# Kernel tuning notes

Measured on AMD Instinct MI355X. Metric: run time of the kernel, lower is better.

Reference implementation:

```python
import math
import jax, jax.numpy as jnp
import numpy as np

M, D, NL, H, DFF = 14, 128, 2, 4, 512
BS = 256
DK = D // H


def setup_inputs() -> dict:
    key = jax.random.key(0)
    ks = iter(jax.random.split(key, 40))
    def w(shape, s=0.02):
        return jax.random.normal(next(ks), shape, jnp.float32) * s
    return dict(
        src=jax.random.normal(next(ks), (BS, M), jnp.float32),
        t=5,
        fc_w=w((D, 1, 3), 0.3), fc_b=jnp.zeros((D,), jnp.float32),
        gc_w=w((D, 1, 3), 0.3), gc_b=jnp.zeros((D,), jnp.float32),
        ln_w=jnp.ones((D,), jnp.float32), ln_b=jnp.zeros((D,), jnp.float32),
        qw=w((NL, D, D)), qb=jnp.zeros((NL, D), jnp.float32),
        kw=w((NL, D, D)), kb=jnp.zeros((NL, D), jnp.float32),
        vw=w((NL, D, D)), vb=jnp.zeros((NL, D), jnp.float32),
        ow=w((NL, D, D)), ob=jnp.zeros((NL, D), jnp.float32),
        n1a=jnp.ones((NL, D), jnp.float32), n1b=jnp.zeros((NL, D), jnp.float32),
        n2a=jnp.ones((NL, D), jnp.float32), n2b=jnp.zeros((NL, D), jnp.float32),
        w1=w((NL, DFF, D)), b1=jnp.zeros((NL, DFF), jnp.float32),
        w2=w((NL, D, DFF)), b2=jnp.zeros((NL, D), jnp.float32),
        fna=jnp.ones((D,), jnp.float32), fnb=jnp.zeros((D,), jnp.float32),
        out_w=w((1, D)), out_b=jnp.zeros((1,), jnp.float32),
    )


def _conv1d(x, w):  # x [B,1,m], w [O,1,3], padding=1 (SAME)
    return jax.lax.conv_general_dilated(
        x, w, window_strides=(1,), padding=[(1, 1)],
        dimension_numbers=('NCH', 'OIH', 'NCH'))


def _norm(x, a, b, eps=1e-6):
    # torch: alpha*(x-mean)/(std+eps)+bias, std is UNBIASED (ddof=1)
    mu = x.mean(-1, keepdims=True)
    std = jnp.sqrt(jnp.var(x, axis=-1, ddof=1, keepdims=True))
    return a * (x - mu) / (std + eps) + b


def _mha(x, qw, qb, kw, kb, vw, vb, ow, ob):
    bs = x.shape[0]
    def proj(w, b):  # view(bs,-1,h,dk).transpose(1,2) -> [bs,h,s,dk]
        return jnp.swapaxes((x @ w.T + b).reshape(bs, -1, H, DK), 1, 2)
    q, k, v = proj(qw, qb), proj(kw, kb), proj(vw, vb)
    scores = jax.nn.softmax(
        jnp.einsum('bhqd,bhkd->bhqk', q, k) / math.sqrt(DK), axis=-1)
    o = jnp.einsum('bhqk,bhkd->bhqd', scores, v)
    o = jnp.swapaxes(o, 1, 2).reshape(bs, -1, D)
    return o @ ow.T + ob


def _forward(src, fc_w, fc_b, gc_w, gc_b, ln_w, ln_b, qw, qb, kw, kb, vw, vb,
             ow, ob, n1a, n1b, n2a, n2b, w1, b1, w2, b2, fna, fnb,
             out_w, out_b, t):
    # --- GCU embedding: gated conv over the m features, pooled to [bs, D]
    xc = src[:, None, :]                                 # [bs,1,m]
    feat = _conv1d(xc, fc_w) + fc_b[None, :, None]        # [bs,D,m]
    gate = jax.nn.sigmoid(_conv1d(xc, gc_w) + gc_b[None, :, None])
    g = (feat * gate).mean(-1)                            # adaptive_avg_pool1d(.,1)
    mu = g.mean(-1, keepdims=True)                        # torch LayerNorm (biased var)
    var = ((g - mu) ** 2).mean(-1, keepdims=True)
    x = ln_w * (g - mu) / jnp.sqrt(var + 1e-5) + ln_b     # [bs,D]
    # --- positional encoding with scalar position t
    div = jnp.exp(jnp.arange(0, D, 2, dtype=jnp.float32) * (-math.log(10000.0) / D))
    pe = jnp.zeros((D,), jnp.float32).at[0::2].set(jnp.sin(t * div)).at[1::2].set(jnp.cos(t * div))
    x = x * math.sqrt(D) + pe
    # --- encoder layers (layer 0 broadcast-promotes x to [bs,bs,D], faithful to torch)
    for i in range(NL):
        x2 = _norm(x, n1a[i], n1b[i])
        x = x + _mha(x2, qw[i], qb[i], kw[i], kb[i], vw[i], vb[i], ow[i], ob[i])
        x2 = _norm(x, n2a[i], n2b[i])
        x = x + (jax.nn.relu(x2 @ w1[i].T + b1[i]) @ w2[i].T + b2[i])
    x = _norm(x, fna, fnb)
    out = x @ out_w.T + out_b                             # [bs,bs,1]
    return out.squeeze(-1)                                # [bs,bs]


def reference(src, fc_w, fc_b, gc_w, gc_b, ln_w, ln_b, qw, qb, kw, kb, vw, vb,
              ow, ob, n1a, n1b, n2a, n2b, w1, b1, w2, b2, fna, fnb,
              out_w, out_b, t):
    return _forward(src, fc_w, fc_b, gc_w, gc_b, ln_w, ln_b, qw, qb, kw, kb,
                    vw, vb, ow, ob, n1a, n1b, n2a, n2b, w1, b1, w2, b2,
                    fna, fnb, out_w, out_b, t)
```

## Files before the change

### kernel.cpp

```cpp
#include <hip/hip_runtime.h>
#include <math.h>


#define SQRT_D 11.313708498984761f
#define PE_C   0.14391156831212787f
#define INV_SQRT_DK 0.17677669529663687f
#define XF(j,d) (((j) << 7) + ((d) ^ (((j) & 15) << 2)))

typedef _Float16 f16x8 __attribute__((ext_vector_type(8)));
typedef float    f32x4 __attribute__((ext_vector_type(4)));

#define MFMA(a, b, c) __builtin_amdgcn_mfma_f32_16x16x32_f16((a), (b), (c), 0, 0, 0)

__device__ __forceinline__ unsigned pack2(float a, float b) {
  union { _Float16 h; unsigned short s; } ua, ub;
  ua.h = (_Float16)a; ub.h = (_Float16)b;
  return (unsigned)ua.s | ((unsigned)ub.s << 16);
}

__device__ __forceinline__ unsigned bperm(int addr, unsigned v) {
  return (unsigned)__builtin_amdgcn_ds_bpermute(addr, (int)v);
}

__device__ __forceinline__ f16x8 u4f16x8(unsigned u0, unsigned u1, unsigned u2, unsigned u3) {
  union { unsigned u[4]; f16x8 f; } x;
  x.u[0] = u0; x.u[1] = u1; x.u[2] = u2; x.u[3] = u3;
  return x.f;
}

__device__ __forceinline__ f16x8 make_bfrag(f32x4 cA, f32x4 cB, int aLo, int aHi, int hiSel) {
  unsigned a0 = pack2(cA[0], cA[1]), a1 = pack2(cA[2], cA[3]);
  unsigned b0 = pack2(cB[0], cB[1]), b1 = pack2(cB[2], cB[3]);
  unsigned lA0 = bperm(aLo, a0), lA1 = bperm(aLo, a1);
  unsigned hA0 = bperm(aHi, a0), hA1 = bperm(aHi, a1);
  unsigned lB0 = bperm(aLo, b0), lB1 = bperm(aLo, b1);
  unsigned hB0 = bperm(aHi, b0), hB1 = bperm(aHi, b1);
  return u4f16x8(hiSel ? lB0 : lA0, hiSel ? lB1 : lA1,
                 hiSel ? hB0 : hA0, hiSel ? hB1 : hA1);
}

struct P0 { const float *qw, *kw, *vw, *ow, *w1, *w2; _Float16* dst; };

__global__ __launch_bounds__(256) void convf16(P0 p) {
  const int idx = blockIdx.x * 256 + threadIdx.x;
  float v;
  if      (idx <  32768) v = p.qw[idx];
  else if (idx <  65536) v = p.kw[idx -  32768];
  else if (idx <  98304) v = p.vw[idx -  65536];
  else if (idx < 131072) v = p.ow[idx -  98304];
  else if (idx < 262144) v = p.w1[idx - 131072];
  else                   v = p.w2[idx - 262144];
  p.dst[idx] = (_Float16)v;
}

struct P1 {
  const float* src; const int* t;
  const float* fc_w; const float* fc_b; const float* gc_w; const float* gc_b;
  const float* ln_w; const float* ln_b;
  const float* n1a; const float* n1b;
  const float* vw; const float* vb; const float* ow; const float* ob;
  float* x0; float* a0;
};

__device__ __forceinline__ float rowReduceSum(float v, volatile float* red, int d) {
#pragma unroll
  for (int off = 32; off > 0; off >>= 1) v += __shfl_xor(v, off, 64);
  if ((d & 63) == 0) red[d >> 6] = v;
  __syncthreads();
  float r = red[0] + red[1];
  __syncthreads();
  return r;
}

__device__ __forceinline__ float dot128s(const float* __restrict__ w,
                                         const float* __restrict__ xs) {
  const float4* __restrict__ w4 = (const float4*)w;
  const float4* __restrict__ x4 = (const float4*)xs;
  float a0 = 0.f, a1 = 0.f, a2 = 0.f, a3 = 0.f;
#pragma unroll
  for (int k = 0; k < 32; k += 4) {
    float4 xv0 = x4[k + 0], xv1 = x4[k + 1], xv2 = x4[k + 2], xv3 = x4[k + 3];
    float4 wv0 = w4[k + 0], wv1 = w4[k + 1], wv2 = w4[k + 2], wv3 = w4[k + 3];
    a0 = fmaf(wv0.w, xv0.w, fmaf(wv0.z, xv0.z, fmaf(wv0.y, xv0.y, fmaf(wv0.x, xv0.x, a0))));
    a1 = fmaf(wv1.w, xv1.w, fmaf(wv1.z, xv1.z, fmaf(wv1.y, xv1.y, fmaf(wv1.x, xv1.x, a1))));
    a2 = fmaf(wv2.w, xv2.w, fmaf(wv2.z, xv2.z, fmaf(wv2.y, xv2.y, fmaf(wv2.x, xv2.x, a2))));
    a3 = fmaf(wv3.w, xv3.w, fmaf(wv3.z, xv3.z, fmaf(wv3.y, xv3.y, fmaf(wv3.x, xv3.x, a3))));
  }
  return (a0 + a1) + (a2 + a3);
}

__global__ __launch_bounds__(256) void prep(P1 p) {
  __shared__ __align__(16) float s_src[2][16];
  __shared__ __align__(16) float s_x2[2][128];
  __shared__ __align__(16) float s_y[2][128];
  __shared__ float s_red[2][2];

  const int tid = threadIdx.x;
  const int rl  = tid >> 7;
  const int d   = tid & 127;
  const int row = blockIdx.x * 2 + rl;
  volatile float* red = s_red[rl];

  if (d < 14) s_src[rl][d + 1] = p.src[row * 14 + d];
  if (d == 14) { s_src[rl][0] = 0.f; s_src[rl][15] = 0.f; }
  __syncthreads();

  const float fw0 = p.fc_w[3*d+0], fw1 = p.fc_w[3*d+1], fw2 = p.fc_w[3*d+2];
  const float gw0 = p.gc_w[3*d+0], gw1 = p.gc_w[3*d+1], gw2 = p.gc_w[3*d+2];
  const float fb = p.fc_b[d], gb = p.gc_b[d];
  float g = 0.f;
#pragma unroll
  for (int m = 0; m < 14; ++m) {
    float xm1 = s_src[rl][m], x0v = s_src[rl][m+1], xp1 = s_src[rl][m+2];
    float f  = fmaf(fw2, xp1, fmaf(fw1, x0v, fmaf(fw0, xm1, fb)));
    float ga = fmaf(gw2, xp1, fmaf(gw1, x0v, fmaf(gw0, xm1, gb)));
    g = fmaf(f, 1.f / (1.f + expf(-ga)), g);
  }
  g *= (1.f / 14.f);

  float mu = rowReduceSum(g, red, d) * (1.f / 128.f);
  float cg = g - mu;
  float var = rowReduceSum(cg * cg, red, d) * (1.f / 128.f);
  float x = fmaf(p.ln_w[d], cg * rsqrtf(var + 1e-5f), p.ln_b[d]);

  const int tval = *p.t;
  {
    int i2 = d >> 1;
    float arg = (float)tval * expf((float)i2 * -PE_C);
    float pe = (d & 1) ? cosf(arg) : sinf(arg);
    x = fmaf(x, SQRT_D, pe);
  }
  p.x0[row * 128 + d] = x;

  float mu1 = rowReduceSum(x, red, d) * (1.f / 128.f);
  float c1 = x - mu1;
  float v1 = rowReduceSum(c1 * c1, red, d) * (1.f / 127.f);
  s_x2[rl][d] = fmaf(p.n1a[d], c1 / (sqrtf(v1) + 1e-6f), p.n1b[d]);
  __syncthreads();

  float y = p.vb[d] + dot128s(p.vw + d * 128, s_x2[rl]);
  s_y[rl][d] = y;
  __syncthreads();
  p.a0[row * 128 + d] = p.ob[d] + dot128s(p.ow + d * 128, s_y[rl]);
}

struct P2 {
  const float* x0; const float* a0;
  const _Float16 *wq, *wk, *wvv, *wo, *w1h, *w2h;
  const float *qb, *kb, *vb, *ob;
  const float *n1a, *n1b, *n2a, *n2b;
  const float *b1, *b2;
  const float *fna, *fnb, *out_w, *out_b;
  float* out;
};

__device__ __forceinline__ void build_x2_pass(const float* sX, int strip, int nt, int l,
    const float* __restrict__ na, const float* __restrict__ nb, f16x8 out[4]) {
  const int l15 = l & 15, q = l >> 4;
  const int row = strip + nt * 16 + l15;
  float sum = 0.f, sq = 0.f;
#pragma unroll
  for (int c4 = 0; c4 < 8; ++c4) {
    f32x4 v = *(const f32x4*)&sX[XF(row, q * 32 + c4 * 4)];
#pragma unroll
    for (int e = 0; e < 4; ++e) { sum += v[e]; sq = fmaf(v[e], v[e], sq); }
  }
  sum += __shfl_xor(sum, 16); sum += __shfl_xor(sum, 32);
  sq  += __shfl_xor(sq, 16);  sq  += __shfl_xor(sq, 32);
  const float mu = sum * (1.f / 128.f);
  const float var = fmaf(-sum, mu, sq) * (1.f / 127.f);
  const float inv = 1.f / (sqrtf(var) + 1e-6f);
#pragma unroll
  for (int kt = 0; kt < 4; ++kt) {
    const int d0 = kt * 32 + q * 8;
    f32x4 xA = *(const f32x4*)&sX[XF(row, d0)];
    f32x4 xB = *(const f32x4*)&sX[XF(row, d0 + 4)];
    f32x4 nA = *(const f32x4*)&na[d0], nB = *(const f32x4*)&na[d0 + 4];
    f32x4 bA = *(const f32x4*)&nb[d0], bB = *(const f32x4*)&nb[d0 + 4];
    float v0 = fmaf(nA[0] * inv, xA[0] - mu, bA[0]);
    float v1 = fmaf(nA[1] * inv, xA[1] - mu, bA[1]);
    float v2 = fmaf(nA[2] * inv, xA[2] - mu, bA[2]);
    float v3 = fmaf(nA[3] * inv, xA[3] - mu, bA[3]);
    float v4 = fmaf(nB[0] * inv, xB[0] - mu, bB[0]);
    float v5 = fmaf(nB[1] * inv, xB[1] - mu, bB[1]);
    float v6 = fmaf(nB[2] * inv, xB[2] - mu, bB[2]);
    float v7 = fmaf(nB[3] * inv, xB[3] - mu, bB[3]);
    out[kt] = u4f16x8(pack2(v0, v1), pack2(v2, v3), pack2(v4, v5), pack2(v6, v7));
  }
}

__device__ __forceinline__ void ffn_phase(float* sX, _Float16* aux, int t,
    int strip, int l, const float* __restrict__ na, const float* __restrict__ nb,
    const _Float16* __restrict__ w1, const float* __restrict__ b1,
    const _Float16* __restrict__ w2, const float* __restrict__ b2,
    int aLo, int aHi, int hiSel) {
  const int l15 = l & 15, lg = l >> 4;
  f16x8 x2f[4][2];
#pragma unroll
  for (int nt = 0; nt < 2; ++nt) {
    f16x8 tmp[4];
    build_x2_pass(sX, strip, nt, l, na, nb, tmp);
#pragma unroll
    for (int kt = 0; kt < 4; ++kt) x2f[kt][nt] = tmp[kt];
  }
  const int sr1 = t >> 4, sg1 = t & 15;
  const int sr2 = t >> 3, sg2 = t & 7;
#pragma unroll 1
  for (int c = 0; c < 8; ++c) {
    __syncthreads();
#pragma unroll
    for (int r = 0; r < 2; ++r) {
      const int row = r * 32 + sr1;
      f16x8 v = *(const f16x8*)(w1 + (c * 64 + row) * 128 + sg1 * 8);
      *(f16x8*)(aux + row * 128 + ((sg1 ^ (row & 15)) << 3)) = v;
    }
#pragma unroll
    for (int r = 0; r < 2; ++r) {
      const int row = r * 64 + sr2;
      f16x8 v = *(const f16x8*)(w2 + row * 512 + c * 64 + sg2 * 8);
      *(f16x8*)(aux + 8192 + row * 64 + ((sg2 ^ (row & 7)) << 3)) = v;
    }
    __syncthreads();
    f32x4 hacc[4][2];
#pragma unroll
    for (int mt = 0; mt < 4; ++mt) {
      f32x4 b = *(const f32x4*)&b1[c * 64 + mt * 16 + lg * 4];
      hacc[mt][0] = b; hacc[mt][1] = b;
    }
#pragma unroll
    for (int mt = 0; mt < 4; ++mt)
#pragma unroll
      for (int kt = 0; kt < 4; ++kt) {
        f16x8 a = *(const f16x8*)(aux + (mt * 16 + l15) * 128 + (((kt * 4 + lg) ^ l15) << 3));
        hacc[mt][0] = MFMA(a, x2f[kt][0], hacc[mt][0]);
        hacc[mt][1] = MFMA(a, x2f[kt][1], hacc[mt][1]);
      }
#pragma unroll
    for (int mt = 0; mt < 4; ++mt)
#pragma unroll
      for (int nt = 0; nt < 2; ++nt)
#pragma unroll
        for (int e = 0; e < 4; ++e) hacc[mt][nt][e] = fmaxf(hacc[mt][nt][e], 0.f);
    f16x8 hf[2][2];
#pragma unroll
    for (int kt2 = 0; kt2 < 2; ++kt2) {
      hf[kt2][0] = make_bfrag(hacc[kt2 * 2][0], hacc[kt2 * 2 + 1][0], aLo, aHi, hiSel);
      hf[kt2][1] = make_bfrag(hacc[kt2 * 2][1], hacc[kt2 * 2 + 1][1], aLo, aHi, hiSel);
    }
#pragma unroll 1
    for (int dh = 0; dh < 2; ++dh) {
      f32x4 oacc[4][2];
#pragma unroll
      for (int mt = 0; mt < 4; ++mt) {
        if (c == 0) {
          f32x4 b = *(const f32x4*)&b2[dh * 64 + mt * 16 + lg * 4];
          oacc[mt][0] = b; oacc[mt][1] = b;
        } else {
          f32x4 z = {0.f, 0.f, 0.f, 0.f};
          oacc[mt][0] = z; oacc[mt][1] = z;
        }
      }
#pragma unroll
      for (int kt2 = 0; kt2 < 2; ++kt2)
#pragma unroll
        for (int mt = 0; mt < 4; ++mt) {
          const int row = dh * 64 + mt * 16 + l15;
          f16x8 a = *(const f16x8*)(aux + 8192 + row * 64 + (((kt2 * 4 + lg) ^ (l15 & 7)) << 3));
          oacc[mt][0] = MFMA(a, hf[kt2][0], oacc[mt][0]);
          oacc[mt][1] = MFMA(a, hf[kt2][1], oacc[mt][1]);
        }
#pragma unroll
      for (int mt = 0; mt < 4; ++mt)
#pragma unroll
        for (int nt = 0; nt < 2; ++nt) {
          const int row = strip + nt * 16 + l15;
          float* dst = &sX[XF(row, dh * 64 + mt * 16 + lg * 4)];
          f32x4 v = *(const f32x4*)dst;
          v += oacc[mt][nt];
          *(f32x4*)dst = v;
        }
    }
  }
}

__global__ __launch_bounds__(512) void batchk(P2 p) {
  __shared__ __align__(16) float sX[32768];
  __shared__ __align__(16) _Float16 sAux[16384];

  const int t = threadIdx.x;
  const int i = blockIdx.x;
  const int l = t & 63;
  const int wv = t >> 6;
  const int strip = wv * 32;
  const int l15 = l & 15;
  const int lg = l >> 4;
  const int hiSel = (l >> 5) & 1;
  const int aLo = ((((lg & 1) * 2 + 0) * 16) + l15) * 4;
  const int aHi = ((((lg & 1) * 2 + 1) * 16) + l15) * 4;

  {
    const int j = t >> 1, hf = t & 1;
    const float* xr = p.x0 + j * 128 + hf * 64;
    const float* ar = p.a0 + i * 128 + hf * 64;
#pragma unroll
    for (int c = 0; c < 16; ++c) {
      f32x4 a = *(const f32x4*)(xr + c * 4);
      f32x4 b = *(const f32x4*)(ar + c * 4);
      a += b;
      *(f32x4*)&sX[XF(j, hf * 64 + c * 4)] = a;
    }
  }

  ffn_phase(sX, sAux, t, strip, l, p.n2a, p.n2b, p.w1h, p.b1, p.w2h, p.b2,
            aLo, aHi, hiSel);

  {
    const _Float16* __restrict__ qw = p.wq + 16384;
    const _Float16* __restrict__ kw = p.wk + 16384;
    const _Float16* __restrict__ vw = p.wvv + 16384;
    const _Float16* __restrict__ ow = p.wo + 16384;
    const float* __restrict__ qb1 = p.qb + 128;
    const float* __restrict__ kb1 = p.kb + 128;
    const float* __restrict__ vb1 = p.vb + 128;
    const float* __restrict__ ob1 = p.ob + 128;

    f16x8 x2f[4][2];
#pragma unroll
    for (int nt = 0; nt < 2; ++nt) {
      f16x8 tmp[4];
      build_x2_pass(sX, strip, nt, l, p.n1a + 128, p.n1b + 128, tmp);
#pragma unroll
      for (int kt = 0; kt < 4; ++kt) x2f[kt][nt] = tmp[kt];
    }

    const int sr = t >> 4, sg = t & 15;

#pragma unroll 1
    for (int h = 0; h < 4; ++h) {
      __syncthreads();
      {
        f16x8 v0 = *(const f16x8*)(kw + (h * 32 + sr) * 128 + sg * 8);
        *(f16x8*)(sAux + sr * 128 + ((sg ^ (sr & 15)) << 3)) = v0;
        f16x8 v1 = *(const f16x8*)(vw + (h * 32 + sr) * 128 + sg * 8);
        *(f16x8*)(sAux + 4096 + sr * 128 + ((sg ^ (sr & 15)) << 3)) = v1;
        f16x8 v2 = *(const f16x8*)(qw + (h * 32 + sr) * 128 + sg * 8);
        *(f16x8*)(sAux + 8192 + sr * 128 + ((sg ^ (sr & 15)) << 3)) = v2;
      }
      __syncthreads();

      f32x4 kacc[2][2], vacc[2][2], qacc[2][2];
#pragma unroll
      for (int mt = 0; mt < 2; ++mt) {
        f32x4 kb4 = *(const f32x4*)&kb1[h * 32 + mt * 16 + lg * 4];
        f32x4 vb4 = *(const f32x4*)&vb1[h * 32 + mt * 16 + lg * 4];
        f32x4 qb4 = *(const f32x4*)&qb1[h * 32 + mt * 16 + lg * 4];
        kacc[mt][0] = kb4; kacc[mt][1] = kb4;
        vacc[mt][0] = vb4; vacc[mt][1] = vb4;
        qacc[mt][0] = qb4; qacc[mt][1] = qb4;
      }
#pragma unroll
      for (int mt = 0; mt < 2; ++mt)
#pragma unroll
        for (int kt = 0; kt < 4; ++kt) {
          const int off = (mt * 16 + l15) * 128 + (((kt * 4 + lg) ^ l15) << 3);
          f16x8 ak = *(const f16x8*)(sAux + off);
          f16x8 av = *(const f16x8*)(sAux + 4096 + off);
          f16x8 aq = *(const f16x8*)(sAux + 8192 + off);
          kacc[mt][0] = MFMA(ak, x2f[kt][0], kacc[mt][0]);
          kacc[mt][1] = MFMA(ak, x2f[kt][1], kacc[mt][1]);
          vacc[mt][0] = MFMA(av, x2f[kt][0], vacc[mt][0]);
          vacc[mt][1] = MFMA(av, x2f[kt][1], vacc[mt][1]);
          qacc[mt][0] = MFMA(aq, x2f[kt][0], qacc[mt][0]);
          qacc[mt][1] = MFMA(aq, x2f[kt][1], qacc[mt][1]);
        }
#pragma unroll
      for (int mt = 0; mt < 2; ++mt)
#pragma unroll
        for (int nt = 0; nt < 2; ++nt)
#pragma unroll
          for (int e = 0; e < 4; ++e) qacc[mt][nt][e] *= INV_SQRT_DK;
      f16x8 qf[2];
      qf[0] = make_bfrag(qacc[0][0], qacc[1][0], aLo, aHi, hiSel);
      qf[1] = make_bfrag(qacc[0][1], qacc[1][1], aLo, aHi, hiSel);
      __syncthreads();

#pragma unroll
      for (int mt = 0; mt < 2; ++mt)
#pragma unroll
        for (int nt = 0; nt < 2; ++nt) {
          const int j = strip + nt * 16 + l15;
          const int db = mt * 16 + lg * 4;
          uint2 w;
          w.x = pack2(kacc[mt][nt][0], kacc[mt][nt][1]);
          w.y = pack2(kacc[mt][nt][2], kacc[mt][nt][3]);
          *(uint2*)(sAux + j * 32 + (db ^ ((j & 3) << 3))) = w;
#pragma unroll
          for (int e = 0; e < 4; ++e) {
            const int d = mt * 16 + lg * 4 + e;
            sAux[8192 + d * 256 + (j ^ ((d & 7) << 3))] = (_Float16)vacc[mt][nt][e];
          }
        }
      __syncthreads();

#pragma unroll
      for (int nt = 0; nt < 2; ++nt) {
        float mrun = -3e38f, lsum = 0.f;
        f32x4 oacc[2];
        { f32x4 z = {0.f, 0.f, 0.f, 0.f}; oacc[0] = z; oacc[1] = z; }
#pragma unroll 1
        for (int ktile = 0; ktile < 8; ++ktile) {
          f32x4 sacc[2];
#pragma unroll
          for (int mt2 = 0; mt2 < 2; ++mt2) {
            const int k = ktile * 32 + mt2 * 16 + l15;
            f16x8 a = *(const f16x8*)(sAux + k * 32 + ((lg * 8) ^ ((k & 3) << 3)));
            f32x4 z = {0.f, 0.f, 0.f, 0.f};
            sacc[mt2] = MFMA(a, qf[nt], z);
          }
          float tm = -3e38f;
#pragma unroll
          for (int mt2 = 0; mt2 < 2; ++mt2)
#pragma unroll
            for (int e = 0; e < 4; ++e) tm = fmaxf(tm, sacc[mt2][e]);
          tm = fmaxf(tm, __shfl_xor(tm, 16));
          tm = fmaxf(tm, __shfl_xor(tm, 32));
          const float mnew = fmaxf(mrun, tm);
          const float corr = __expf(mrun - mnew);
          float ts = 0.f;
#pragma unroll
          for (int mt2 = 0; mt2 < 2; ++mt2)
#pragma unroll
            for (int e = 0; e < 4; ++e) {
              float ev = __expf(sacc[mt2][e] - mnew);
              sacc[mt2][e] = ev;
              ts += ev;
            }
          ts += __shfl_xor(ts, 16);
          ts += __shfl_xor(ts, 32);
          lsum = fmaf(lsum, corr, ts);
          oacc[0] *= corr; oacc[1] *= corr;
          f16x8 pf = make_bfrag(sacc[0], sacc[1], aLo, aHi, hiSel);
#pragma unroll
          for (int mt2 = 0; mt2 < 2; ++mt2) {
            const int d = mt2 * 16 + l15;
            f16x8 a = *(const f16x8*)(sAux + 8192 + d * 256 + ((ktile * 32 + lg * 8) ^ ((d & 7) << 3)));
            oacc[mt2] = MFMA(a, pf, oacc[mt2]);
          }
          mrun = mnew;
        }
        const float linv = 1.f / lsum;
        oacc[0] *= linv; oacc[1] *= linv;
        f16x8 of = make_bfrag(oacc[0], oacc[1], aLo, aHi, hiSel);
        f32x4 zacc[8];
#pragma unroll
        for (int mt = 0; mt < 8; ++mt) {
          if (h == 0) zacc[mt] = *(const f32x4*)&ob1[mt * 16 + lg * 4];
          else { f32x4 z = {0.f, 0.f, 0.f, 0.f}; zacc[mt] = z; }
        }
#pragma unroll
        for (int mt = 0; mt < 8; ++mt) {
          f16x8 a = *(const f16x8*)(ow + (mt * 16 + l15) * 128 + h * 32 + lg * 8);
          zacc[mt] = MFMA(a, of, zacc[mt]);
        }
        const int row = strip + nt * 16 + l15;
#pragma unroll
        for (int mt = 0; mt < 8; ++mt) {
          float* dst = &sX[XF(row, mt * 16 + lg * 4)];
          f32x4 v = *(const f32x4*)dst;
          v += zacc[mt];
          *(f32x4*)dst = v;
        }
      }
    }
  }

  ffn_phase(sX, sAux, t, strip, l, p.n2a + 128, p.n2b + 128,
            p.w1h + 65536, p.b1 + 512, p.w2h + 65536, p.b2 + 128,
            aLo, aHi, hiSel);

  {
    const int r = strip + (l & 31), hf = l >> 5;
    float sum = 0.f, sq = 0.f;
#pragma unroll
    for (int c = 0; c < 16; ++c) {
      f32x4 v = *(const f32x4*)&sX[XF(r, hf * 64 + c * 4)];
#pragma unroll
      for (int e = 0; e < 4; ++e) { sum += v[e]; sq = fmaf(v[e], v[e], sq); }
    }
    sum += __shfl_xor(sum, 32);
    sq  += __shfl_xor(sq, 32);
    float mu = sum * (1.f / 128.f);
    float var = fmaf(-sum, mu, sq) * (1.f / 127.f);
    float inv = 1.f / (sqrtf(var) + 1e-6f);
    float os = 0.f;
#pragma unroll
    for (int c = 0; c < 16; ++c) {
      f32x4 x  = *(const f32x4*)&sX[XF(r, hf * 64 + c * 4)];
      f32x4 fa = *(const f32x4*)&p.fna[hf * 64 + c * 4];
      f32x4 fb = *(const f32x4*)&p.fnb[hf * 64 + c * 4];
      f32x4 wo = *(const f32x4*)&p.out_w[hf * 64 + c * 4];
#pragma unroll
      for (int e = 0; e < 4; ++e)
        os = fmaf(fmaf(fa[e] * inv, x[e] - mu, fb[e]), wo[e], os);
    }
    os += __shfl_xor(os, 32);
    if (l < 32) p.out[i * 256 + r] = os + p.out_b[0];
  }
}

extern "C" void kernel_launch(void* const* d_in, const int* in_sizes, int n_in,
                              void* d_out, int out_size, void* d_ws, size_t ws_size,
                              hipStream_t stream) {
  float* x0 = (float*)d_ws;
  float* a0 = x0 + 32768;
  _Float16* W16 = (_Float16*)((char*)d_ws + 262144);

  P0 p0;
  p0.qw = (const float*)d_in[8];  p0.kw = (const float*)d_in[10];
  p0.vw = (const float*)d_in[12]; p0.ow = (const float*)d_in[14];
  p0.w1 = (const float*)d_in[20]; p0.w2 = (const float*)d_in[22];
  p0.dst = W16;
  convf16<<<dim3(1536), dim3(256), 0, stream>>>(p0);

  P1 p1;
  p1.src  = (const float*)d_in[0];
  p1.t    = (const int*)  d_in[1];
  p1.fc_w = (const float*)d_in[2];  p1.fc_b = (const float*)d_in[3];
  p1.gc_w = (const float*)d_in[4];  p1.gc_b = (const float*)d_in[5];
  p1.ln_w = (const float*)d_in[6];  p1.ln_b = (const float*)d_in[7];
  p1.n1a  = (const float*)d_in[16]; p1.n1b  = (const float*)d_in[17];
  p1.vw   = (const float*)d_in[12]; p1.vb   = (const float*)d_in[13];
  p1.ow   = (const float*)d_in[14]; p1.ob   = (const float*)d_in[15];
  p1.x0 = x0; p1.a0 = a0;
  prep<<<dim3(128), dim3(256), 0, stream>>>(p1);

  P2 p2;
  p2.x0 = x0; p2.a0 = a0;
  p2.wq  = W16;
  p2.wk  = W16 + 32768;
  p2.wvv = W16 + 65536;
  p2.wo  = W16 + 98304;
  p2.w1h = W16 + 131072;
  p2.w2h = W16 + 262144;
  p2.qb = (const float*)d_in[9];  p2.kb = (const float*)d_in[11];
  p2.vb = (const float*)d_in[13]; p2.ob = (const float*)d_in[15];
  p2.n1a = (const float*)d_in[16]; p2.n1b = (const float*)d_in[17];
  p2.n2a = (const float*)d_in[18]; p2.n2b = (const float*)d_in[19];
  p2.b1 = (const float*)d_in[21];  p2.b2 = (const float*)d_in[23];
  p2.fna = (const float*)d_in[24]; p2.fnb = (const float*)d_in[25];
  p2.out_w = (const float*)d_in[26]; p2.out_b = (const float*)d_in[27];
  p2.out = (float*)d_out;
  batchk<<<dim3(256), dim3(512), 0, stream>>>(p2);
}
```

Before: 142.1 us.

## Double threads per block so each wave owns a 16-row strip

The batch kernel moves from 512 to 1024 threads (16 waves). Each wave now handles 16 rows instead of 32, so the per-wave accumulator arrays lose their second column tile. Weight staging is split across the larger thread count. The aim is more latency hiding and lower per-thread register pressure, at the cost of more waves contending for barriers and less reuse of each A-fragment loaded from LDS per MFMA.

```diff
diff --git a/kernel.cpp b/kernel.cpp
--- a/kernel.cpp
+++ b/kernel.cpp
@@ -154,10 +154,10 @@
   float* out;
 };
 
-__device__ __forceinline__ void build_x2_pass(const float* sX, int strip, int nt, int l,
+__device__ __forceinline__ void build_x2_pass(const float* sX, int strip, int l,
     const float* __restrict__ na, const float* __restrict__ nb, f16x8 out[4]) {
   const int l15 = l & 15, q = l >> 4;
-  const int row = strip + nt * 16 + l15;
+  const int row = strip + l15;
   float sum = 0.f, sq = 0.f;
 #pragma unroll
   for (int c4 = 0; c4 < 8; ++c4) {
@@ -195,70 +195,48 @@
     const _Float16* __restrict__ w2, const float* __restrict__ b2,
     int aLo, int aHi, int hiSel) {
   const int l15 = l & 15, lg = l >> 4;
-  f16x8 x2f[4][2];
-#pragma unroll
-  for (int nt = 0; nt < 2; ++nt) {
-    f16x8 tmp[4];
-    build_x2_pass(sX, strip, nt, l, na, nb, tmp);
-#pragma unroll
-    for (int kt = 0; kt < 4; ++kt) x2f[kt][nt] = tmp[kt];
-  }
+  f16x8 x2f[4];
+  build_x2_pass(sX, strip, l, na, nb, x2f);
   const int sr1 = t >> 4, sg1 = t & 15;
   const int sr2 = t >> 3, sg2 = t & 7;
 #pragma unroll 1
   for (int c = 0; c < 8; ++c) {
     __syncthreads();
-#pragma unroll
-    for (int r = 0; r < 2; ++r) {
-      const int row = r * 32 + sr1;
-      f16x8 v = *(const f16x8*)(w1 + (c * 64 + row) * 128 + sg1 * 8);
-      *(f16x8*)(aux + row * 128 + ((sg1 ^ (row & 15)) << 3)) = v;
-    }
-#pragma unroll
-    for (int r = 0; r < 2; ++r) {
-      const int row = r * 64 + sr2;
-      f16x8 v = *(const f16x8*)(w2 + row * 512 + c * 64 + sg2 * 8);
-      *(f16x8*)(aux + 8192 + row * 64 + ((sg2 ^ (row & 7)) << 3)) = v;
+    {
+      f16x8 v = *(const f16x8*)(w1 + (c * 64 + sr1) * 128 + sg1 * 8);
+      *(f16x8*)(aux + sr1 * 128 + ((sg1 ^ (sr1 & 15)) << 3)) = v;
+    }
+    {
+      f16x8 v = *(const f16x8*)(w2 + sr2 * 512 + c * 64 + sg2 * 8);
+      *(f16x8*)(aux + 8192 + sr2 * 64 + ((sg2 ^ (sr2 & 7)) << 3)) = v;
     }
     __syncthreads();
-    f32x4 hacc[4][2];
-#pragma unroll
-    for (int mt = 0; mt < 4; ++mt) {
-      f32x4 b = *(const f32x4*)&b1[c * 64 + mt * 16 + lg * 4];
-      hacc[mt][0] = b; hacc[mt][1] = b;
-    }
+    f32x4 hacc[4];
+#pragma unroll
+    for (int mt = 0; mt < 4; ++mt)
+      hacc[mt] = *(const f32x4*)&b1[c * 64 + mt * 16 + lg * 4];
 #pragma unroll
     for (int mt = 0; mt < 4; ++mt)
 #pragma unroll
       for (int kt = 0; kt < 4; ++kt) {
         f16x8 a = *(const f16x8*)(aux + (mt * 16 + l15) * 128 + (((kt * 4 + lg) ^ l15) << 3));
-        hacc[mt][0] = MFMA(a, x2f[kt][0], hacc[mt][0]);
-        hacc[mt][1] = MFMA(a, x2f[kt][1], hacc[mt][1]);
+        hacc[mt] = MFMA(a, x2f[kt], hacc[mt]);
       }
 #pragma unroll
     for (int mt = 0; mt < 4; ++mt)
 #pragma unroll
-      for (int nt = 0; nt < 2; ++nt)
-#pragma unroll
-        for (int e = 0; e < 4; ++e) hacc[mt][nt][e] = fmaxf(hacc[mt][nt][e], 0.f);
-    f16x8 hf[2][2];
-#pragma unroll
-    for (int kt2 = 0; kt2 < 2; ++kt2) {
-      hf[kt2][0] = make_bfrag(hacc[kt2 * 2][0], hacc[kt2 * 2 + 1][0], aLo, aHi, hiSel);
-      hf[kt2][1] = make_bfrag(hacc[kt2 * 2][1], hacc[kt2 * 2 + 1][1], aLo, aHi, hiSel);
-    }
+      for (int e = 0; e < 4; ++e) hacc[mt][e] = fmaxf(hacc[mt][e], 0.f);
+    f16x8 hf[2];
+#pragma unroll
+    for (int kt2 = 0; kt2 < 2; ++kt2)
+      hf[kt2] = make_bfrag(hacc[kt2 * 2], hacc[kt2 * 2 + 1], aLo, aHi, hiSel);
 #pragma unroll 1
     for (int dh = 0; dh < 2; ++dh) {
-      f32x4 oacc[4][2];
+      f32x4 oacc[4];
 #pragma unroll
       for (int mt = 0; mt < 4; ++mt) {
-        if (c == 0) {
-          f32x4 b = *(const f32x4*)&b2[dh * 64 + mt * 16 + lg * 4];
-          oacc[mt][0] = b; oacc[mt][1] = b;
-        } else {
-          f32x4 z = {0.f, 0.f, 0.f, 0.f};
-          oacc[mt][0] = z; oacc[mt][1] = z;
-        }
+        if (c == 0) oacc[mt] = *(const f32x4*)&b2[dh * 64 + mt * 16 + lg * 4];
+        else { f32x4 z = {0.f, 0.f, 0.f, 0.f}; oacc[mt] = z; }
       }
 #pragma unroll
       for (int kt2 = 0; kt2 < 2; ++kt2)
@@ -266,24 +244,21 @@
         for (int mt = 0; mt < 4; ++mt) {
           const int row = dh * 64 + mt * 16 + l15;
           f16x8 a = *(const f16x8*)(aux + 8192 + row * 64 + (((kt2 * 4 + lg) ^ (l15 & 7)) << 3));
-          oacc[mt][0] = MFMA(a, hf[kt2][0], oacc[mt][0]);
-          oacc[mt][1] = MFMA(a, hf[kt2][1], oacc[mt][1]);
+          oacc[mt] = MFMA(a, hf[kt2], oacc[mt]);
         }
 #pragma unroll
-      for (int mt = 0; mt < 4; ++mt)
-#pragma unroll
-        for (int nt = 0; nt < 2; ++nt) {
-          const int row = strip + nt * 16 + l15;
-          float* dst = &sX[XF(row, dh * 64 + mt * 16 + lg * 4)];
-          f32x4 v = *(const f32x4*)dst;
-          v += oacc[mt][nt];
-          *(f32x4*)dst = v;
-        }
-    }
-  }
-}
-
-__global__ __launch_bounds__(512) void batchk(P2 p) {
+      for (int mt = 0; mt < 4; ++mt) {
+        const int row = strip + l15;
+        float* dst = &sX[XF(row, dh * 64 + mt * 16 + lg * 4)];
+        f32x4 v = *(const f32x4*)dst;
+        v += oacc[mt];
+        *(f32x4*)dst = v;
+      }
+    }
+  }
+}
+
+__global__ __launch_bounds__(1024) void batchk(P2 p) {
   __shared__ __align__(16) float sX[32768];
   __shared__ __align__(16) _Float16 sAux[16384];
 
@@ -291,7 +266,7 @@
   const int i = blockIdx.x;
   const int l = t & 63;
   const int wv = t >> 6;
-  const int strip = wv * 32;
+  const int strip = wv * 16;
   const int l15 = l & 15;
   const int lg = l >> 4;
   const int hiSel = (l >> 5) & 1;
@@ -299,15 +274,15 @@
   const int aHi = ((((lg & 1) * 2 + 1) * 16) + l15) * 4;
 
   {
-    const int j = t >> 1, hf = t & 1;
-    const float* xr = p.x0 + j * 128 + hf * 64;
-    const float* ar = p.a0 + i * 128 + hf * 64;
-#pragma unroll
-    for (int c = 0; c < 16; ++c) {
+    const int j = t >> 2, q = t & 3;
+    const float* xr = p.x0 + j * 128 + q * 32;
+    const float* ar = p.a0 + i * 128 + q * 32;
+#pragma unroll
+    for (int c = 0; c < 8; ++c) {
       f32x4 a = *(const f32x4*)(xr + c * 4);
       f32x4 b = *(const f32x4*)(ar + c * 4);
       a += b;
-      *(f32x4*)&sX[XF(j, hf * 64 + c * 4)] = a;
+      *(f32x4*)&sX[XF(j, q * 32 + c * 4)] = a;
     }
   }
 
@@ -324,39 +299,31 @@
     const float* __restrict__ vb1 = p.vb + 128;
     const float* __restrict__ ob1 = p.ob + 128;
 
-    f16x8 x2f[4][2];
-#pragma unroll
-    for (int nt = 0; nt < 2; ++nt) {
-      f16x8 tmp[4];
-      build_x2_pass(sX, strip, nt, l, p.n1a + 128, p.n1b + 128, tmp);
-#pragma unroll
-      for (int kt = 0; kt < 4; ++kt) x2f[kt][nt] = tmp[kt];
-    }
-
-    const int sr = t >> 4, sg = t & 15;
+    f16x8 x2f[4];
+    build_x2_pass(sX, strip, l, p.n1a + 128, p.n1b + 128, x2f);
+
+    const int sr = (t & 511) >> 4, sg = t & 15;
 
 #pragma unroll 1
     for (int h = 0; h < 4; ++h) {
       __syncthreads();
-      {
+      if (t < 512) {
         f16x8 v0 = *(const f16x8*)(kw + (h * 32 + sr) * 128 + sg * 8);
         *(f16x8*)(sAux + sr * 128 + ((sg ^ (sr & 15)) << 3)) = v0;
         f16x8 v1 = *(const f16x8*)(vw + (h * 32 + sr) * 128 + sg * 8);
         *(f16x8*)(sAux + 4096 + sr * 128 + ((sg ^ (sr & 15)) << 3)) = v1;
+      } else {
         f16x8 v2 = *(const f16x8*)(qw + (h * 32 + sr) * 128 + sg * 8);
         *(f16x8*)(sAux + 8192 + sr * 128 + ((sg ^ (sr & 15)) << 3)) = v2;
       }
       __syncthreads();
 
-      f32x4 kacc[2][2], vacc[2][2], qacc[2][2];
+      f32x4 kacc[2], vacc[2], qacc[2];
 #pragma unroll
       for (int mt = 0; mt < 2; ++mt) {
-        f32x4 kb4 = *(const f32x4*)&kb1[h * 32 + mt * 16 + lg * 4];
-        f32x4 vb4 = *(const f32x4*)&vb1[h * 32 + mt * 16 + lg * 4];
-        f32x4 qb4 = *(const f32x4*)&qb1[h * 32 + mt * 16 + lg * 4];
-        kacc[mt][0] = kb4; kacc[mt][1] = kb4;
-        vacc[mt][0] = vb4; vacc[mt][1] = vb4;
-        qacc[mt][0] = qb4; qacc[mt][1] = qb4;
+        kacc[mt] = *(const f32x4*)&kb1[h * 32 + mt * 16 + lg * 4];
+        vacc[mt] = *(const f32x4*)&vb1[h * 32 + mt * 16 + lg * 4];
+        qacc[mt] = *(const f32x4*)&qb1[h * 32 + mt * 16 + lg * 4];
       }
 #pragma unroll
       for (int mt = 0; mt < 2; ++mt)
@@ -366,110 +333,98 @@
           f16x8 ak = *(const f16x8*)(sAux + off);
           f16x8 av = *(const f16x8*)(sAux + 4096 + off);
           f16x8 aq = *(const f16x8*)(sAux + 8192 + off);
-          kacc[mt][0] = MFMA(ak, x2f[kt][0], kacc[mt][0]);
-          kacc[mt][1] = MFMA(ak, x2f[kt][1], kacc[mt][1]);
-          vacc[mt][0] = MFMA(av, x2f[kt][0], vacc[mt][0]);
-          vacc[mt][1] = MFMA(av, x2f[kt][1], vacc[mt][1]);
-          qacc[mt][0] = MFMA(aq, x2f[kt][0], qacc[mt][0]);
-          qacc[mt][1] = MFMA(aq, x2f[kt][1], qacc[mt][1]);
+          kacc[mt] = MFMA(ak, x2f[kt], kacc[mt]);
+          vacc[mt] = MFMA(av, x2f[kt], vacc[mt]);
+          qacc[mt] = MFMA(aq, x2f[kt], qacc[mt]);
         }
 #pragma unroll
       for (int mt = 0; mt < 2; ++mt)
 #pragma unroll
-        for (int nt = 0; nt < 2; ++nt)
-#pragma unroll
-          for (int e = 0; e < 4; ++e) qacc[mt][nt][e] *= INV_SQRT_DK;
-      f16x8 qf[2];
-      qf[0] = make_bfrag(qacc[0][0], qacc[1][0], aLo, aHi, hiSel);
-      qf[1] = make_bfrag(qacc[0][1], qacc[1][1], aLo, aHi, hiSel);
+        for (int e = 0; e < 4; ++e) qacc[mt][e] *= INV_SQRT_DK;
+      f16x8 qf = make_bfrag(qacc[0], qacc[1], aLo, aHi, hiSel);
       __syncthreads();
 
 #pragma unroll
-      for (int mt = 0; mt < 2; ++mt)
-#pragma unroll
-        for (int nt = 0; nt < 2; ++nt) {
-          const int j = strip + nt * 16 + l15;
-          const int db = mt * 16 + lg * 4;
-          uint2 w;
-          w.x = pack2(kacc[mt][nt][0], kacc[mt][nt][1]);
-          w.y = pack2(kacc[mt][nt][2], kacc[mt][nt][3]);
-          *(uint2*)(sAux + j * 32 + (db ^ ((j & 3) << 3))) = w;
+      for (int mt = 0; mt < 2; ++mt) {
+        const int j = strip + l15;
+        const int db = mt * 16 + lg * 4;
+        uint2 w;
+        w.x = pack2(kacc[mt][0], kacc[mt][1]);
+        w.y = pack2(kacc[mt][2], kacc[mt][3]);
+        *(uint2*)(sAux + j * 32 + (db ^ ((j & 3) << 3))) = w;
+#pragma unroll
+        for (int e = 0; e < 4; ++e) {
+          const int d = mt * 16 + lg * 4 + e;
+          sAux[8192 + d * 256 + (j ^ ((d & 7) << 3))] = (_Float16)vacc[mt][e];
+        }
+      }
+      __syncthreads();
+
+      float mrun = -3e38f, lsum = 0.f;
+      f32x4 oacc[2];
+      { f32x4 z = {0.f, 0.f, 0.f, 0.f}; oacc[0] = z; oacc[1] = z; }
+#pragma unroll 1
+      for (int ktile = 0; ktile < 8; ++ktile) {
+        f32x4 sacc[2];
+#pragma unroll
+        for (int mt2 = 0; mt2 < 2; ++mt2) {
+          const int k = ktile * 32 + mt2 * 16 + l15;
+          f16x8 a = *(const f16x8*)(sAux + k * 32 + ((lg * 8) ^ ((k & 3) << 3)));
+          f32x4 z = {0.f, 0.f, 0.f, 0.f};
+          sacc[mt2] = MFMA(a, qf, z);
+        }
+        float tm = -3e38f;
+#pragma unroll
+        for (int mt2 = 0; mt2 < 2; ++mt2)
+#pragma unroll
+          for (int e = 0; e < 4; ++e) tm = fmaxf(tm, sacc[mt2][e]);
+        tm = fmaxf(tm, __shfl_xor(tm, 16));
+        tm = fmaxf(tm, __shfl_xor(tm, 32));
+        const float mnew = fmaxf(mrun, tm);
+        const float corr = __expf(mrun - mnew);
+        float ts = 0.f;
+#pragma unroll
+        for (int mt2 = 0; mt2 < 2; ++mt2)
 #pragma unroll
           for (int e = 0; e < 4; ++e) {
-            const int d = mt * 16 + lg * 4 + e;
-            sAux[8192 + d * 256 + (j ^ ((d & 7) << 3))] = (_Float16)vacc[mt][nt][e];
+            float ev = __expf(sacc[mt2][e] - mnew);
+            sacc[mt2][e] = ev;
+            ts += ev;
           }
+        ts += __shfl_xor(ts, 16);
+        ts += __shfl_xor(ts, 32);
+        lsum = fmaf(lsum, corr, ts);
+        oacc[0] *= corr; oacc[1] *= corr;
+        f16x8 pf = make_bfrag(sacc[0], sacc[1], aLo, aHi, hiSel);
+#pragma unroll
+        for (int mt2 = 0; mt2 < 2; ++mt2) {
+          const int d = mt2 * 16 + l15;
+          f16x8 a = *(const f16x8*)(sAux + 8192 + d * 256 + ((ktile * 32 + lg * 8) ^ ((d & 7) << 3)));
+          oacc[mt2] = MFMA(a, pf, oacc[mt2]);
         }
-      __syncthreads();
-
-#pragma unroll
-      for (int nt = 0; nt < 2; ++nt) {
-        float mrun = -3e38f, lsum = 0.f;
-        f32x4 oacc[2];
-        { f32x4 z = {0.f, 0.f, 0.f, 0.f}; oacc[0] = z; oacc[1] = z; }
-#pragma unroll 1
-        for (int ktile = 0; ktile < 8; ++ktile) {
-          f32x4 sacc[2];
-#pragma unroll
-          for (int mt2 = 0; mt2 < 2; ++mt2) {
-            const int k = ktile * 32 + mt2 * 16 + l15;
-            f16x8 a = *(const f16x8*)(sAux + k * 32 + ((lg * 8) ^ ((k & 3) << 3)));
-            f32x4 z = {0.f, 0.f, 0.f, 0.f};
-            sacc[mt2] = MFMA(a, qf[nt], z);
-          }
-          float tm = -3e38f;
-#pragma unroll
-          for (int mt2 = 0; mt2 < 2; ++mt2)
-#pragma unroll
-            for (int e = 0; e < 4; ++e) tm = fmaxf(tm, sacc[mt2][e]);
-          tm = fmaxf(tm, __shfl_xor(tm, 16));
-          tm = fmaxf(tm, __shfl_xor(tm, 32));
-          const float mnew = fmaxf(mrun, tm);
-          const float corr = __expf(mrun - mnew);
-          float ts = 0.f;
-#pragma unroll
-          for (int mt2 = 0; mt2 < 2; ++mt2)
-#pragma unroll
-            for (int e = 0; e < 4; ++e) {
-              float ev = __expf(sacc[mt2][e] - mnew);
-              sacc[mt2][e] = ev;
-              ts += ev;
-            }
-          ts += __shfl_xor(ts, 16);
-          ts += __shfl_xor(ts, 32);
-          lsum = fmaf(lsum, corr, ts);
-          oacc[0] *= corr; oacc[1] *= corr;
-          f16x8 pf = make_bfrag(sacc[0], sacc[1], aLo, aHi, hiSel);
-#pragma unroll
-          for (int mt2 = 0; mt2 < 2; ++mt2) {
-            const int d = mt2 * 16 + l15;
-            f16x8 a = *(const f16x8*)(sAux + 8192 + d * 256 + ((ktile * 32 + lg * 8) ^ ((d & 7) << 3)));
-            oacc[mt2] = MFMA(a, pf, oacc[mt2]);
-          }
-          mrun = mnew;
-        }
-        const float linv = 1.f / lsum;
-        oacc[0] *= linv; oacc[1] *= linv;
-        f16x8 of = make_bfrag(oacc[0], oacc[1], aLo, aHi, hiSel);
-        f32x4 zacc[8];
-#pragma unroll
-        for (int mt = 0; mt < 8; ++mt) {
-          if (h == 0) zacc[mt] = *(const f32x4*)&ob1[mt * 16 + lg * 4];
-          else { f32x4 z = {0.f, 0.f, 0.f, 0.f}; zacc[mt] = z; }
-        }
-#pragma unroll
-        for (int mt = 0; mt < 8; ++mt) {
-          f16x8 a = *(const f16x8*)(ow + (mt * 16 + l15) * 128 + h * 32 + lg * 8);
-          zacc[mt] = MFMA(a, of, zacc[mt]);
-        }
-        const int row = strip + nt * 16 + l15;
-#pragma unroll
-        for (int mt = 0; mt < 8; ++mt) {
-          float* dst = &sX[XF(row, mt * 16 + lg * 4)];
-          f32x4 v = *(const f32x4*)dst;
-          v += zacc[mt];
-          *(f32x4*)dst = v;
-        }
+        mrun = mnew;
+      }
+      const float linv = 1.f / lsum;
+      oacc[0] *= linv; oacc[1] *= linv;
+      f16x8 of = make_bfrag(oacc[0], oacc[1], aLo, aHi, hiSel);
+      f32x4 zacc[8];
+#pragma unroll
+      for (int mt = 0; mt < 8; ++mt) {
+        if (h == 0) zacc[mt] = *(const f32x4*)&ob1[mt * 16 + lg * 4];
+        else { f32x4 z = {0.f, 0.f, 0.f, 0.f}; zacc[mt] = z; }
+      }
+#pragma unroll
+      for (int mt = 0; mt < 8; ++mt) {
+        f16x8 a = *(const f16x8*)(ow + (mt * 16 + l15) * 128 + h * 32 + lg * 8);
+        zacc[mt] = MFMA(a, of, zacc[mt]);
+      }
+      const int row = strip + l15;
+#pragma unroll
+      for (int mt = 0; mt < 8; ++mt) {
+        float* dst = &sX[XF(row, mt * 16 + lg * 4)];
+        f32x4 v = *(const f32x4*)dst;
+        v += zacc[mt];
+        *(f32x4*)dst = v;
       }
     }
   }
@@ -479,32 +434,32 @@
             aLo, aHi, hiSel);
 
   {
-    const int r = strip + (l & 31), hf = l >> 5;
+    const int r = strip + l15, q = lg;
     float sum = 0.f, sq = 0.f;
 #pragma unroll
-    for (int c = 0; c < 16; ++c) {
-      f32x4 v = *(const f32x4*)&sX[XF(r, hf * 64 + c * 4)];
+    for (int c = 0; c < 8; ++c) {
+      f32x4 v = *(const f32x4*)&sX[XF(r, q * 32 + c * 4)];
 #pragma unroll
       for (int e = 0; e < 4; ++e) { sum += v[e]; sq = fmaf(v[e], v[e], sq); }
     }
-    sum += __shfl_xor(sum, 32);
-    sq  += __shfl_xor(sq, 32);
+    sum += __shfl_xor(sum, 16); sum += __shfl_xor(sum, 32);
+    sq  += __shfl_xor(sq, 16);  sq  += __shfl_xor(sq, 32);
     float mu = sum * (1.f / 128.f);
     float var = fmaf(-sum, mu, sq) * (1.f / 127.f);
     float inv = 1.f / (sqrtf(var) + 1e-6f);
     float os = 0.f;
 #pragma unroll
-    for (int c = 0; c < 16; ++c) {
-      f32x4 x  = *(const f32x4*)&sX[XF(r, hf * 64 + c * 4)];
-      f32x4 fa = *(const f32x4*)&p.fna[hf * 64 + c * 4];
-      f32x4 fb = *(const f32x4*)&p.fnb[hf * 64 + c * 4];
-      f32x4 wo = *(const f32x4*)&p.out_w[hf * 64 + c * 4];
+    for (int c = 0; c < 8; ++c) {
+      f32x4 x  = *(const f32x4*)&sX[XF(r, q * 32 + c * 4)];
+      f32x4 fa = *(const f32x4*)&p.fna[q * 32 + c * 4];
+      f32x4 fb = *(const f32x4*)&p.fnb[q * 32 + c * 4];
+      f32x4 wo = *(const f32x4*)&p.out_w[q * 32 + c * 4];
 #pragma unroll
       for (int e = 0; e < 4; ++e)
         os = fmaf(fmaf(fa[e] * inv, x[e] - mu, fb[e]), wo[e], os);
     }
-    os += __shfl_xor(os, 32);
-    if (l < 32) p.out[i * 256 + r] = os + p.out_b[0];
+    os += __shfl_xor(os, 16); os += __shfl_xor(os, 32);
+    if (l < 16) p.out[i * 256 + r] = os + p.out_b[0];
   }
 }
 
@@ -550,5 +505,5 @@
   p2.fna = (const float*)d_in[24]; p2.fnb = (const float*)d_in[25];
   p2.out_w = (const float*)d_in[26]; p2.out_b = (const float*)d_in[27];
   p2.out = (float*)d_out;
-  batchk<<<dim3(256), dim3(512), 0, stream>>>(p2);
-}
+  batchk<<<dim3(256), dim3(1024), 0, stream>>>(p2);
+}
```

Result: slower. 155.8 us (+9.6%).

## Pre-swizzle fp16 weights and double-buffer FFN weight staging with register prefetch

Applied to the files above, without the earlier changes.

The conversion kernel now writes weights in a pre-swizzled, chunk-contiguous fp16 layout, and drops the unused layer-0 Q/K/V/O copies. The in-kernel loads become plain linear 16-byte copies into shared memory. The FFN loop uses 32-row chunks with two LDS buffers and prefetches the next chunk into registers while the current one is computed, which removes one barrier per iteration. It also adds s_setprio around the MFMA sections, at the cost of twice as many loop iterations and more index arithmetic in the conversion kernel.

```diff
diff --git a/kernel.cpp b/kernel.cpp
--- a/kernel.cpp
+++ b/kernel.cpp
@@ -41,16 +41,37 @@
 
 struct P0 { const float *qw, *kw, *vw, *ow, *w1, *w2; _Float16* dst; };
 
-__global__ __launch_bounds__(256) void convf16(P0 p) {
-  const int idx = blockIdx.x * 256 + threadIdx.x;
-  float v;
-  if      (idx <  32768) v = p.qw[idx];
-  else if (idx <  65536) v = p.kw[idx -  32768];
-  else if (idx <  98304) v = p.vw[idx -  65536];
-  else if (idx < 131072) v = p.ow[idx -  98304];
-  else if (idx < 262144) v = p.w1[idx - 131072];
-  else                   v = p.w2[idx - 262144];
-  p.dst[idx] = (_Float16)v;
+__global__ __launch_bounds__(256) void convswz(P0 p) {
+  const int i = blockIdx.x * 256 + threadIdx.x;
+  const float* src; int sidx;
+  if (i < 262144) {
+    const int L = i >> 17;
+    const int r = i & 131071;
+    if (r < 65536) {
+      const int c = (r >> 12) & 15, row = (r >> 7) & 31, gs = (r >> 3) & 15, e = r & 7;
+      const int g = gs ^ (row & 15);
+      sidx = L * 65536 + (c * 32 + row) * 128 + g * 8 + e;
+      src = p.w1;
+    } else {
+      const int j = r - 65536;
+      const int c = (j >> 12) & 15, row = (j >> 5) & 127, gs = (j >> 3) & 3, e = j & 7;
+      const int g = gs ^ (row & 3);
+      sidx = L * 65536 + row * 512 + c * 32 + g * 8 + e;
+      src = p.w2;
+    }
+  } else if (i < 311296) {
+    const int j = i - 262144;
+    const int m = j >> 14;
+    const int rem = j & 16383;
+    const int h = (rem >> 12) & 3, row = (rem >> 7) & 31, gs = (rem >> 3) & 15, e = rem & 7;
+    const int g = gs ^ (row & 15);
+    sidx = 16384 + (h * 32 + row) * 128 + g * 8 + e;
+    src = (m == 0) ? p.kw : ((m == 1) ? p.vw : p.qw);
+  } else {
+    sidx = 16384 + (i - 311296);
+    src = p.ow;
+  }
+  p.dst[i] = (_Float16)src[sidx];
 }
 
 struct P1 {
@@ -146,7 +167,9 @@
 
 struct P2 {
   const float* x0; const float* a0;
-  const _Float16 *wq, *wk, *wvv, *wo, *w1h, *w2h;
+  const _Float16* wff;
+  const _Float16* wkvq;
+  const _Float16* wow;
   const float *qb, *kb, *vb, *ob;
   const float *n1a, *n1b, *n2a, *n2b;
   const float *b1, *b2;
@@ -191,8 +214,8 @@
 
 __device__ __forceinline__ void ffn_phase(float* sX, _Float16* aux, int t,
     int strip, int l, const float* __restrict__ na, const float* __restrict__ nb,
-    const _Float16* __restrict__ w1, const float* __restrict__ b1,
-    const _Float16* __restrict__ w2, const float* __restrict__ b2,
+    const _Float16* __restrict__ w1s, const float* __restrict__ b1,
+    const _Float16* __restrict__ w2s, const float* __restrict__ b2,
     int aLo, int aHi, int hiSel) {
   const int l15 = l & 15, lg = l >> 4;
   f16x8 x2f[4][2];
@@ -203,50 +226,44 @@
 #pragma unroll
     for (int kt = 0; kt < 4; ++kt) x2f[kt][nt] = tmp[kt];
   }
-  const int sr1 = t >> 4, sg1 = t & 15;
-  const int sr2 = t >> 3, sg2 = t & 7;
+  f16x8 pre1 = *(const f16x8*)(w1s + t * 8);
+  f16x8 pre2 = *(const f16x8*)(w2s + t * 8);
+  __syncthreads();
 #pragma unroll 1
-  for (int c = 0; c < 8; ++c) {
+  for (int c = 0; c < 16; ++c) {
+    _Float16* buf = aux + (c & 1) * 8192;
+    *(f16x8*)(buf + t * 8) = pre1;
+    *(f16x8*)(buf + 4096 + t * 8) = pre2;
     __syncthreads();
-#pragma unroll
-    for (int r = 0; r < 2; ++r) {
-      const int row = r * 32 + sr1;
-      f16x8 v = *(const f16x8*)(w1 + (c * 64 + row) * 128 + sg1 * 8);
-      *(f16x8*)(aux + row * 128 + ((sg1 ^ (row & 15)) << 3)) = v;
-    }
-#pragma unroll
-    for (int r = 0; r < 2; ++r) {
-      const int row = r * 64 + sr2;
-      f16x8 v = *(const f16x8*)(w2 + row * 512 + c * 64 + sg2 * 8);
-      *(f16x8*)(aux + 8192 + row * 64 + ((sg2 ^ (row & 7)) << 3)) = v;
-    }
-    __syncthreads();
-    f32x4 hacc[4][2];
-#pragma unroll
-    for (int mt = 0; mt < 4; ++mt) {
-      f32x4 b = *(const f32x4*)&b1[c * 64 + mt * 16 + lg * 4];
+    if (c < 15) {
+      pre1 = *(const f16x8*)(w1s + (c + 1) * 4096 + t * 8);
+      pre2 = *(const f16x8*)(w2s + (c + 1) * 4096 + t * 8);
+    }
+    f32x4 hacc[2][2];
+#pragma unroll
+    for (int mt = 0; mt < 2; ++mt) {
+      f32x4 b = *(const f32x4*)&b1[c * 32 + mt * 16 + lg * 4];
       hacc[mt][0] = b; hacc[mt][1] = b;
     }
-#pragma unroll
-    for (int mt = 0; mt < 4; ++mt)
+    __builtin_amdgcn_s_setprio(1);
+#pragma unroll
+    for (int mt = 0; mt < 2; ++mt)
 #pragma unroll
       for (int kt = 0; kt < 4; ++kt) {
-        f16x8 a = *(const f16x8*)(aux + (mt * 16 + l15) * 128 + (((kt * 4 + lg) ^ l15) << 3));
+        f16x8 a = *(const f16x8*)(buf + (mt * 16 + l15) * 128 + (((kt * 4 + lg) ^ l15) << 3));
         hacc[mt][0] = MFMA(a, x2f[kt][0], hacc[mt][0]);
         hacc[mt][1] = MFMA(a, x2f[kt][1], hacc[mt][1]);
       }
-#pragma unroll
-    for (int mt = 0; mt < 4; ++mt)
+    __builtin_amdgcn_s_setprio(0);
+#pragma unroll
+    for (int mt = 0; mt < 2; ++mt)
 #pragma unroll
       for (int nt = 0; nt < 2; ++nt)
 #pragma unroll
         for (int e = 0; e < 4; ++e) hacc[mt][nt][e] = fmaxf(hacc[mt][nt][e], 0.f);
-    f16x8 hf[2][2];
-#pragma unroll
-    for (int kt2 = 0; kt2 < 2; ++kt2) {
-      hf[kt2][0] = make_bfrag(hacc[kt2 * 2][0], hacc[kt2 * 2 + 1][0], aLo, aHi, hiSel);
-      hf[kt2][1] = make_bfrag(hacc[kt2 * 2][1], hacc[kt2 * 2 + 1][1], aLo, aHi, hiSel);
-    }
+    f16x8 hf0 = make_bfrag(hacc[0][0], hacc[1][0], aLo, aHi, hiSel);
+    f16x8 hf1 = make_bfrag(hacc[0][1], hacc[1][1], aLo, aHi, hiSel);
+    const _Float16* w2c = buf + 4096;
 #pragma unroll 1
     for (int dh = 0; dh < 2; ++dh) {
       f32x4 oacc[4][2];
@@ -260,15 +277,15 @@
           oacc[mt][0] = z; oacc[mt][1] = z;
         }
       }
-#pragma unroll
-      for (int kt2 = 0; kt2 < 2; ++kt2)
-#pragma unroll
-        for (int mt = 0; mt < 4; ++mt) {
-          const int row = dh * 64 + mt * 16 + l15;
-          f16x8 a = *(const f16x8*)(aux + 8192 + row * 64 + (((kt2 * 4 + lg) ^ (l15 & 7)) << 3));
-          oacc[mt][0] = MFMA(a, hf[kt2][0], oacc[mt][0]);
-          oacc[mt][1] = MFMA(a, hf[kt2][1], oacc[mt][1]);
-        }
+      __builtin_amdgcn_s_setprio(1);
+#pragma unroll
+      for (int mt = 0; mt < 4; ++mt) {
+        const int row = dh * 64 + mt * 16 + l15;
+        f16x8 a = *(const f16x8*)(w2c + row * 32 + ((lg ^ (row & 3)) << 3));
+        oacc[mt][0] = MFMA(a, hf0, oacc[mt][0]);
+        oacc[mt][1] = MFMA(a, hf1, oacc[mt][1]);
+      }
+      __builtin_amdgcn_s_setprio(0);
 #pragma unroll
       for (int mt = 0; mt < 4; ++mt)
 #pragma unroll
@@ -311,14 +328,10 @@
     }
   }
 
-  ffn_phase(sX, sAux, t, strip, l, p.n2a, p.n2b, p.w1h, p.b1, p.w2h, p.b2,
-            aLo, aHi, hiSel);
+  ffn_phase(sX, sAux, t, strip, l, p.n2a, p.n2b, p.wff, p.b1,
+            p.wff + 65536, p.b2, aLo, aHi, hiSel);
 
   {
-    const _Float16* __restrict__ qw = p.wq + 16384;
-    const _Float16* __restrict__ kw = p.wk + 16384;
-    const _Float16* __restrict__ vw = p.wvv + 16384;
-    const _Float16* __restrict__ ow = p.wo + 16384;
     const float* __restrict__ qb1 = p.qb + 128;
     const float* __restrict__ kb1 = p.kb + 128;
     const float* __restrict__ vb1 = p.vb + 128;
@@ -333,19 +346,12 @@
       for (int kt = 0; kt < 4; ++kt) x2f[kt][nt] = tmp[kt];
     }
 
-    const int sr = t >> 4, sg = t & 15;
-
 #pragma unroll 1
     for (int h = 0; h < 4; ++h) {
       __syncthreads();
-      {
-        f16x8 v0 = *(const f16x8*)(kw + (h * 32 + sr) * 128 + sg * 8);
-        *(f16x8*)(sAux + sr * 128 + ((sg ^ (sr & 15)) << 3)) = v0;
-        f16x8 v1 = *(const f16x8*)(vw + (h * 32 + sr) * 128 + sg * 8);
-        *(f16x8*)(sAux + 4096 + sr * 128 + ((sg ^ (sr & 15)) << 3)) = v1;
-        f16x8 v2 = *(const f16x8*)(qw + (h * 32 + sr) * 128 + sg * 8);
-        *(f16x8*)(sAux + 8192 + sr * 128 + ((sg ^ (sr & 15)) << 3)) = v2;
-      }
+      *(f16x8*)(sAux + t * 8)        = *(const f16x8*)(p.wkvq + h * 4096 + t * 8);
+      *(f16x8*)(sAux + 4096 + t * 8) = *(const f16x8*)(p.wkvq + 16384 + h * 4096 + t * 8);
+      *(f16x8*)(sAux + 8192 + t * 8) = *(const f16x8*)(p.wkvq + 32768 + h * 4096 + t * 8);
       __syncthreads();
 
       f32x4 kacc[2][2], vacc[2][2], qacc[2][2];
@@ -358,6 +364,7 @@
         vacc[mt][0] = vb4; vacc[mt][1] = vb4;
         qacc[mt][0] = qb4; qacc[mt][1] = qb4;
       }
+      __builtin_amdgcn_s_setprio(1);
 #pragma unroll
       for (int mt = 0; mt < 2; ++mt)
 #pragma unroll
@@ -373,6 +380,7 @@
           qacc[mt][0] = MFMA(aq, x2f[kt][0], qacc[mt][0]);
           qacc[mt][1] = MFMA(aq, x2f[kt][1], qacc[mt][1]);
         }
+      __builtin_amdgcn_s_setprio(0);
 #pragma unroll
       for (int mt = 0; mt < 2; ++mt)
 #pragma unroll
@@ -457,11 +465,13 @@
           if (h == 0) zacc[mt] = *(const f32x4*)&ob1[mt * 16 + lg * 4];
           else { f32x4 z = {0.f, 0.f, 0.f, 0.f}; zacc[mt] = z; }
         }
+        __builtin_amdgcn_s_setprio(1);
 #pragma unroll
         for (int mt = 0; mt < 8; ++mt) {
-          f16x8 a = *(const f16x8*)(ow + (mt * 16 + l15) * 128 + h * 32 + lg * 8);
+          f16x8 a = *(const f16x8*)(p.wow + (mt * 16 + l15) * 128 + h * 32 + lg * 8);
           zacc[mt] = MFMA(a, of, zacc[mt]);
         }
+        __builtin_amdgcn_s_setprio(0);
         const int row = strip + nt * 16 + l15;
 #pragma unroll
         for (int mt = 0; mt < 8; ++mt) {
@@ -475,7 +485,7 @@
   }
 
   ffn_phase(sX, sAux, t, strip, l, p.n2a + 128, p.n2b + 128,
-            p.w1h + 65536, p.b1 + 512, p.w2h + 65536, p.b2 + 128,
+            p.wff + 131072, p.b1 + 512, p.wff + 196608, p.b2 + 128,
             aLo, aHi, hiSel);
 
   {
@@ -520,7 +530,7 @@
   p0.vw = (const float*)d_in[12]; p0.ow = (const float*)d_in[14];
   p0.w1 = (const float*)d_in[20]; p0.w2 = (const float*)d_in[22];
   p0.dst = W16;
-  convf16<<<dim3(1536), dim3(256), 0, stream>>>(p0);
+  convswz<<<dim3(1280), dim3(256), 0, stream>>>(p0);
 
   P1 p1;
   p1.src  = (const float*)d_in[0];
@@ -536,12 +546,9 @@
 
   P2 p2;
   p2.x0 = x0; p2.a0 = a0;
-  p2.wq  = W16;
-  p2.wk  = W16 + 32768;
-  p2.wvv = W16 + 65536;
-  p2.wo  = W16 + 98304;
-  p2.w1h = W16 + 131072;
-  p2.w2h = W16 + 262144;
+  p2.wff  = W16;
+  p2.wkvq = W16 + 262144;
+  p2.wow  = W16 + 311296;
   p2.qb = (const float*)d_in[9];  p2.kb = (const float*)d_in[11];
   p2.vb = (const float*)d_in[13]; p2.ob = (const float*)d_in[15];
   p2.n1a = (const float*)d_in[16]; p2.n1b = (const float*)d_in[17];
```

After: 163.0 us. +14.7%, slower.
